# Performance work log

Measured on AMD Instinct MI355X. Metric: run time of the kernel, lower is better.

## Reference

```python
import jax, jax.numpy as jnp
import numpy as np

B = 64       # graphs per batch
NPG = 1000   # nodes per graph
EPG = 8000   # edges per graph
F = 128      # num_node_features


def _lin_w(k, fi, fo):
    s = 1.0 / np.sqrt(fi)
    return jax.random.uniform(k, (fi, fo), jnp.float32, -s, s)


def setup_inputs() -> dict:
    key = jax.random.key(0)
    ks = jax.random.split(key, 40)
    N, E = B * NPG, B * EPG

    def edges(k1, k2):
        src = jax.random.randint(k1, (E,), 0, NPG)
        dst = jax.random.randint(k2, (E,), 0, NPG)
        off = (jnp.arange(E) // EPG) * NPG  # keep edges within each graph
        return jnp.stack([src + off, dst + off]).astype(jnp.int32)

    inp = {
        'x0': jax.random.normal(ks[0], (N, F), jnp.float32),
        'edge_attr0': jax.random.uniform(ks[1], (E, 4), jnp.float32),
        'edge_index0': edges(ks[2], ks[3]),
        'x1': jax.random.normal(ks[4], (N, F), jnp.float32),
        'edge_attr1': jax.random.uniform(ks[5], (E, 4), jnp.float32),
        'edge_index1': edges(ks[6], ks[7]),
        'batch0': (jnp.arange(N) // NPG).astype(jnp.int32),
        'batch1': (jnp.arange(N) // NPG).astype(jnp.int32),
        'num_graphs': B,
    }
    # GCNConv weights/biases (6 convs, all F->F)
    names = ['1A', '1B', '1C', '1D', '2', '3']
    for i, nm in enumerate(names):
        inp['W' + nm] = _lin_w(ks[8 + i], F, F)
        inp['b' + nm] = jnp.zeros((F,), jnp.float32)
    # SAGPooling score GNN (GraphConv: lin_rel with bias, lin_root no bias), 3F -> 1
    inp['Ws_rel'] = _lin_w(ks[20], 3 * F, 1)
    inp['bs_rel'] = jnp.zeros((1,), jnp.float32)
    inp['Ws_root'] = _lin_w(ks[21], 3 * F, 1)
    # MLP: 6F -> 32 -> 8 -> 2
    inp['Wm1'] = _lin_w(ks[22], 6 * F, 32)
    inp['bm1'] = jnp.zeros((32,), jnp.float32)
    inp['Wm2'] = _lin_w(ks[23], 32, 8)
    inp['bm2'] = jnp.zeros((8,), jnp.float32)
    inp['Wm3'] = _lin_w(ks[24], 8, 2)
    inp['bm3'] = jnp.zeros((2,), jnp.float32)
    return inp


def gcn_conv(x, W, b, row, col, ew):
    # PyG GCNConv: add self-loops (w=1), symmetric norm, gather->scatter-add
    N = x.shape[0]
    h = x @ W  # [N, F]
    sl = jnp.arange(N)
    row_f = jnp.concatenate([row, sl])
    col_f = jnp.concatenate([col, sl])
    w_f = jnp.concatenate([ew, jnp.ones((N,), x.dtype)])
    deg = jax.ops.segment_sum(w_f, col_f, num_segments=N)
    dinv = jnp.where(deg > 0, jax.lax.rsqrt(jnp.maximum(deg, 1e-12)), 0.0)
    norm = (dinv[row_f] * w_f * dinv[col_f])[:, None]
    return jax.ops.segment_sum(h[row_f] * norm, col_f, num_segments=N) + b


def reference(x0, edge_attr0, edge_index0, x1, edge_attr1, edge_index1,
              batch0, batch1, num_graphs,
              W1A, b1A, W1B, b1B, W1C, b1C, W1D, b1D, W2, b2, W3, b3,
              Ws_rel, bs_rel, Ws_root, Wm1, bm1, Wm2, bm2, Wm3, bm3):
    Bn = int(num_graphs)

    def branch(x, ea, ei):
        row, col = ei[0], ei[1]
        N = x.shape[0]
        ones_e = jnp.ones((ei.shape[1],), x.dtype)
        xa = jax.nn.relu(gcn_conv(x, W1A, b1A, row, col, ea[:, 0]))
        xb = jax.nn.relu(gcn_conv(x, W1B, b1B, row, col, ea[:, 1]))
        xc = jax.nn.relu(gcn_conv(x, W1C, b1C, row, col, ea[:, 2]))
        xd = jax.nn.relu(gcn_conv(x, W1D, b1D, row, col, ea[:, 3]))
        g1 = (xa + xb + xc + xd) * 0.25
        g2 = jax.nn.relu(gcn_conv(g1, W2, b2, row, col, ones_e))
        g3 = gcn_conv(g2, W3, b3, row, col, ones_e)
        g = jnp.concatenate([g1, g2, g3], axis=1)  # [N, 3F]
        # SAGPooling score via GraphConv (sum aggr, no norm/self-loops)
        agg = jax.ops.segment_sum(g[row], col, num_segments=N)
        score = (agg @ Ws_rel + bs_rel + g @ Ws_root)[:, 0]  # [N]
        npg = N // Bn
        k = npg // 2  # ratio=0.5, even graph size
        sv, si = jax.lax.top_k(score.reshape(Bn, npg), k)
        gg = g.reshape(Bn, npg, g.shape[1])
        sel = jnp.take_along_axis(gg, si[..., None], axis=1)  # [B, k, 3F]
        pooled = sel * jnp.tanh(sv)[..., None]
        return pooled.mean(axis=1)  # global_mean_pool -> [B, 3F]

    r0 = branch(x0, edge_attr0, edge_index0)
    r1 = branch(x1, edge_attr1, edge_index1)
    r = jnp.concatenate([r0, r1], axis=1)  # [B, 6F]
    h = jax.nn.relu(r @ Wm1 + bm1)
    h = jax.nn.relu(h @ Wm2 + bm2)
    return h @ Wm3 + bm3  # [B, 2]
```

## Files before the change

kernel.cpp:

```cpp
#include <hip/hip_runtime.h>
#include <math.h>


#define TPB 256

__device__ __forceinline__ int swz_block(int bid, int nb) {
  int per = nb >> 3;
  return (bid & 7) * per + (bid >> 3);
}

__device__ __forceinline__ void f4fma(float4& a, const float4 b, float s) {
  a.x += b.x * s; a.y += b.y * s; a.z += b.z * s; a.w += b.w * s;
}
__device__ __forceinline__ float4 f4s(const float4 a, float s) {
  return make_float4(a.x * s, a.y * s, a.z * s, a.w * s);
}

__global__ __launch_bounds__(TPB) void count_k(const int* __restrict__ col,
                                               int* __restrict__ cnt, int E) {
  int e = blockIdx.x * TPB + threadIdx.x;
  if (e < E) atomicAdd(&cnt[col[e]], 1);
}

__global__ __launch_bounds__(TPB) void scan1_k(const int* __restrict__ cnt,
                                               int* __restrict__ rowptr,
                                               int* __restrict__ bsum, int N) {
  __shared__ int s[TPB];
  int tid = threadIdx.x;
  int gid = blockIdx.x * TPB + tid;
  int v = (gid < N) ? cnt[gid] : 0;
  s[tid] = v;
  __syncthreads();
  for (int o = 1; o < TPB; o <<= 1) {
    int t = (tid >= o) ? s[tid - o] : 0;
    __syncthreads();
    s[tid] += t;
    __syncthreads();
  }
  if (gid < N) rowptr[gid] = s[tid] - v;
  if (tid == TPB - 1) bsum[blockIdx.x] = s[TPB - 1];
}

__global__ __launch_bounds__(TPB) void scan2_k(int* __restrict__ bsum, int nb) {
  __shared__ int s[TPB];
  int tid = threadIdx.x;
  int v = (tid < nb) ? bsum[tid] : 0;
  s[tid] = v;
  __syncthreads();
  for (int o = 1; o < TPB; o <<= 1) {
    int t = (tid >= o) ? s[tid - o] : 0;
    __syncthreads();
    s[tid] += t;
    __syncthreads();
  }
  if (tid < nb) bsum[tid] = s[tid] - v;
}

__global__ __launch_bounds__(TPB) void scan3_k(int* __restrict__ rowptr,
                                               const int* __restrict__ bsum,
                                               int N, int E) {
  int gid = blockIdx.x * TPB + threadIdx.x;
  if (gid < N) rowptr[gid] += bsum[blockIdx.x];
  if (gid == 0) rowptr[N] = E;
}

__global__ __launch_bounds__(TPB) void fill_k(const int* __restrict__ col,
                                              const int* __restrict__ rowptr,
                                              int* __restrict__ fil,
                                              int* __restrict__ csr, int E) {
  int e = blockIdx.x * TPB + threadIdx.x;
  if (e < E) {
    int c = col[e];
    int p = rowptr[c] + atomicAdd(&fil[c], 1);
    csr[p] = e;
  }
}

__global__ __launch_bounds__(TPB) void sortadj_k(const int* __restrict__ rowptr,
                                                 int* __restrict__ csr, int N) {
  int i = blockIdx.x * TPB + threadIdx.x;
  if (i >= N) return;
  int s = rowptr[i], e = rowptr[i + 1];
  for (int a = s + 1; a < e; ++a) {
    int v = csr[a];
    int b = a - 1;
    while (b >= s && csr[b] > v) { csr[b + 1] = csr[b]; --b; }
    csr[b + 1] = v;
  }
}

__global__ __launch_bounds__(TPB) void deg_k(const int* __restrict__ rowptr,
                                             const int* __restrict__ csr,
                                             const float* __restrict__ ea,
                                             float* __restrict__ dinv, int N) {
  int i = blockIdx.x * TPB + threadIdx.x;
  if (i >= N) return;
  int s = rowptr[i], e = rowptr[i + 1];
  float d0 = 1.f, d1 = 1.f, d2 = 1.f, d3 = 1.f;
  for (int j = s; j < e; ++j) {
    int eid = csr[j];
    float4 w = *reinterpret_cast<const float4*>(&ea[(size_t)eid * 4]);
    d0 += w.x; d1 += w.y; d2 += w.z; d3 += w.w;
  }
  float dO = (float)(e - s) + 1.f;
  dinv[0 * N + i] = 1.f / sqrtf(d0);
  dinv[1 * N + i] = 1.f / sqrtf(d1);
  dinv[2 * N + i] = 1.f / sqrtf(d2);
  dinv[3 * N + i] = 1.f / sqrtf(d3);
  dinv[4 * N + i] = 1.f / sqrtf(dO);
}

__global__ __launch_bounds__(TPB) void eresolve_k(
    const int* __restrict__ csr, const int* __restrict__ erow,
    const float* __restrict__ ea, const float* __restrict__ dinv, int N, int E,
    int* __restrict__ csrSrc, float4* __restrict__ csrW,
    float* __restrict__ csrWO) {
  int j = blockIdx.x * TPB + threadIdx.x;
  if (j >= E) return;
  int eid = csr[j];
  int r = erow[eid];
  float4 a = *reinterpret_cast<const float4*>(&ea[(size_t)eid * 4]);
  csrSrc[j] = r;
  csrW[j] = make_float4(a.x * dinv[r], a.y * dinv[N + r], a.z * dinv[2 * N + r],
                        a.w * dinv[3 * N + r]);
  csrWO[j] = dinv[4 * N + r];
}

__global__ __launch_bounds__(256) void gather4_k(
    const float4* __restrict__ X, const int* __restrict__ rowptr,
    const int* __restrict__ csrSrc, const float4* __restrict__ csrW,
    const float* __restrict__ dinv, int N, float4* __restrict__ S0,
    float4* __restrict__ S1, float4* __restrict__ S2, float4* __restrict__ S3) {
  int sb = swz_block(blockIdx.x, gridDim.x);
  int node = sb * 8 + (threadIdx.x >> 5);
  int l = threadIdx.x & 31;
  int s = rowptr[node], e = rowptr[node + 1];
  float d0 = dinv[node], d1 = dinv[N + node], d2 = dinv[2 * N + node],
        d3 = dinv[3 * N + node];
  float4 xs = X[(size_t)node * 32 + l];
  float4 a0 = f4s(xs, d0), a1 = f4s(xs, d1), a2 = f4s(xs, d2), a3 = f4s(xs, d3);
  int j = s;
  for (; j + 3 < e; j += 4) {
    int r0 = csrSrc[j], r1 = csrSrc[j + 1], r2 = csrSrc[j + 2], r3 = csrSrc[j + 3];
    float4 w0 = csrW[j], w1 = csrW[j + 1], w2 = csrW[j + 2], w3 = csrW[j + 3];
    float4 x0 = X[(size_t)r0 * 32 + l];
    float4 x1 = X[(size_t)r1 * 32 + l];
    float4 x2 = X[(size_t)r2 * 32 + l];
    float4 x3 = X[(size_t)r3 * 32 + l];
    f4fma(a0, x0, w0.x); f4fma(a1, x0, w0.y); f4fma(a2, x0, w0.z); f4fma(a3, x0, w0.w);
    f4fma(a0, x1, w1.x); f4fma(a1, x1, w1.y); f4fma(a2, x1, w1.z); f4fma(a3, x1, w1.w);
    f4fma(a0, x2, w2.x); f4fma(a1, x2, w2.y); f4fma(a2, x2, w2.z); f4fma(a3, x2, w2.w);
    f4fma(a0, x3, w3.x); f4fma(a1, x3, w3.y); f4fma(a2, x3, w3.z); f4fma(a3, x3, w3.w);
  }
  for (; j < e; ++j) {
    int r = csrSrc[j];
    float4 w = csrW[j];
    float4 xr = X[(size_t)r * 32 + l];
    f4fma(a0, xr, w.x); f4fma(a1, xr, w.y); f4fma(a2, xr, w.z); f4fma(a3, xr, w.w);
  }
  size_t o = (size_t)node * 32 + l;
  S0[o] = f4s(a0, d0);
  S1[o] = f4s(a1, d1);
  S2[o] = f4s(a2, d2);
  S3[o] = f4s(a3, d3);
}

__global__ __launch_bounds__(256) void gather1_k(
    const float4* __restrict__ X, const int* __restrict__ rowptr,
    const int* __restrict__ csrSrc, const float* __restrict__ csrWO,
    const float* __restrict__ dinvO, int N, float4* __restrict__ Out) {
  int sb = swz_block(blockIdx.x, gridDim.x);
  int node = sb * 8 + (threadIdx.x >> 5);
  int l = threadIdx.x & 31;
  int s = rowptr[node], e = rowptr[node + 1];
  float di = dinvO[node];
  float4 acc = f4s(X[(size_t)node * 32 + l], di);
  int j = s;
  for (; j + 3 < e; j += 4) {
    int r0 = csrSrc[j], r1 = csrSrc[j + 1], r2 = csrSrc[j + 2], r3 = csrSrc[j + 3];
    float w0 = csrWO[j], w1 = csrWO[j + 1], w2 = csrWO[j + 2], w3 = csrWO[j + 3];
    float4 x0 = X[(size_t)r0 * 32 + l];
    float4 x1 = X[(size_t)r1 * 32 + l];
    float4 x2 = X[(size_t)r2 * 32 + l];
    float4 x3 = X[(size_t)r3 * 32 + l];
    f4fma(acc, x0, w0); f4fma(acc, x1, w1); f4fma(acc, x2, w2); f4fma(acc, x3, w3);
  }
  for (; j < e; ++j) {
    f4fma(acc, X[(size_t)csrSrc[j] * 32 + l], csrWO[j]);
  }
  Out[(size_t)node * 32 + l] = f4s(acc, di);
}

#define GEMM_STAGE(Aptr)                                                        \
  {                                                                             \
    _Pragma("unroll")                                                           \
    for (int i = 0; i < 4; ++i) {                                               \
      int u = tid + i * 256;                                                    \
      int r = u >> 3, k4 = u & 7;                                               \
      float4 v = *reinterpret_cast<const float4*>(                              \
          &Aptr[(size_t)(rowBase + r) * 128 + kc + k4 * 4]);                    \
      AsT[k4 * 4 + 0][r] = v.x;                                                 \
      AsT[k4 * 4 + 1][r] = v.y;                                                 \
      AsT[k4 * 4 + 2][r] = v.z;                                                 \
      AsT[k4 * 4 + 3][r] = v.w;                                                 \
    }                                                                           \
    _Pragma("unroll")                                                           \
    for (int i = 0; i < 4; ++i) {                                               \
      int u = tid + i * 256;                                                    \
      int r = u >> 5, c4 = u & 31;                                              \
      *reinterpret_cast<float4*>(&Ws[r][c4 * 4]) =                              \
          *reinterpret_cast<const float4*>(&Wp[(size_t)(kc + r) * 128 + c4 * 4]);\
    }                                                                           \
  }

#define GEMM_COMPUTE()                                                          \
  _Pragma("unroll 8")                                                           \
  for (int k = 0; k < 32; ++k) {                                                \
    float a[8], b[8];                                                           \
    *reinterpret_cast<float4*>(&a[0]) =                                         \
        *reinterpret_cast<const float4*>(&AsT[k][ty * 8]);                      \
    *reinterpret_cast<float4*>(&a[4]) =                                         \
        *reinterpret_cast<const float4*>(&AsT[k][ty * 8 + 4]);                  \
    *reinterpret_cast<float4*>(&b[0]) =                                         \
        *reinterpret_cast<const float4*>(&Ws[k][tx * 8]);                       \
    *reinterpret_cast<float4*>(&b[4]) =                                         \
        *reinterpret_cast<const float4*>(&Ws[k][tx * 8 + 4]);                   \
    _Pragma("unroll")                                                           \
    for (int j = 0; j < 8; ++j) {                                               \
      _Pragma("unroll")                                                         \
      for (int c = 0; c < 8; ++c) acc[j][c] += a[j] * b[c];                     \
    }                                                                           \
  }

template <bool RELU>
__global__ __launch_bounds__(256) void gemm_epi(const float* __restrict__ A,
                                                const float* __restrict__ Wp,
                                                const float* __restrict__ bias,
                                                float* __restrict__ C, int M) {
  __shared__ float AsT[32][132];
  __shared__ float Ws[32][128];
  int tid = threadIdx.x;
  int tx = tid & 15;
  int ty = tid >> 4;
  int rowBase = blockIdx.x * 128;
  float acc[8][8] = {};
  for (int kc = 0; kc < 128; kc += 32) {
    GEMM_STAGE(A);
    __syncthreads();
    GEMM_COMPUTE();
    __syncthreads();
  }
  float bb[8];
  *reinterpret_cast<float4*>(&bb[0]) = *reinterpret_cast<const float4*>(&bias[tx * 8]);
  *reinterpret_cast<float4*>(&bb[4]) = *reinterpret_cast<const float4*>(&bias[tx * 8 + 4]);
#pragma unroll
  for (int j = 0; j < 8; ++j) {
    float o[8];
#pragma unroll
    for (int c = 0; c < 8; ++c) {
      float v = acc[j][c] + bb[c];
      o[c] = RELU ? fmaxf(v, 0.f) : v;
    }
    size_t r = (size_t)(rowBase + ty * 8 + j) * 128 + tx * 8;
    *reinterpret_cast<float4*>(&C[r]) = *reinterpret_cast<float4*>(&o[0]);
    *reinterpret_cast<float4*>(&C[r + 4]) = *reinterpret_cast<float4*>(&o[4]);
  }
}

__global__ __launch_bounds__(256) void gemm4_k(
    const float* __restrict__ S0, const float* __restrict__ S1,
    const float* __restrict__ S2, const float* __restrict__ S3,
    const float* __restrict__ W0, const float* __restrict__ W1,
    const float* __restrict__ W2, const float* __restrict__ W3,
    const float* __restrict__ B0, const float* __restrict__ B1,
    const float* __restrict__ B2, const float* __restrict__ B3,
    float* __restrict__ g1, int M) {
  __shared__ float AsT[32][132];
  __shared__ float Ws[32][128];
  const float* Sarr[4] = {S0, S1, S2, S3};
  const float* Warr[4] = {W0, W1, W2, W3};
  const float* Barr[4] = {B0, B1, B2, B3};
  int tid = threadIdx.x;
  int tx = tid & 15;
  int ty = tid >> 4;
  int rowBase = blockIdx.x * 128;
  float facc[8][8] = {};
  for (int q = 0; q < 4; ++q) {
    const float* A = Sarr[q];
    const float* Wp = Warr[q];
    float acc[8][8] = {};
    for (int kc = 0; kc < 128; kc += 32) {
      GEMM_STAGE(A);
      __syncthreads();
      GEMM_COMPUTE();
      __syncthreads();
    }
    float bb[8];
    *reinterpret_cast<float4*>(&bb[0]) =
        *reinterpret_cast<const float4*>(&Barr[q][tx * 8]);
    *reinterpret_cast<float4*>(&bb[4]) =
        *reinterpret_cast<const float4*>(&Barr[q][tx * 8 + 4]);
#pragma unroll
    for (int j = 0; j < 8; ++j)
#pragma unroll
      for (int c = 0; c < 8; ++c)
        facc[j][c] += fmaxf(acc[j][c] + bb[c], 0.f) * 0.25f;
  }
#pragma unroll
  for (int j = 0; j < 8; ++j) {
    size_t r = (size_t)(rowBase + ty * 8 + j) * 128 + tx * 8;
    *reinterpret_cast<float4*>(&g1[r]) = *reinterpret_cast<float4*>(&facc[j][0]);
    *reinterpret_cast<float4*>(&g1[r + 4]) = *reinterpret_cast<float4*>(&facc[j][4]);
  }
}

__global__ __launch_bounds__(256) void score_a(
    const float* __restrict__ g1, const float* __restrict__ g2,
    const float* __restrict__ g3, const float* __restrict__ Wrel,
    const float* __restrict__ Wroot, float* __restrict__ trel,
    float* __restrict__ troot, int N) {
  int wave = threadIdx.x >> 6;
  int lane = threadIdx.x & 63;
  int node = blockIdx.x * 4 + wave;
  if (node >= N) return;
  float sr = 0.f, so = 0.f;
#pragma unroll
  for (int t = 0; t < 2; ++t) {
    int f = lane + t * 64;
    float v1 = g1[(size_t)node * 128 + f];
    float v2 = g2[(size_t)node * 128 + f];
    float v3 = g3[(size_t)node * 128 + f];
    sr += v1 * Wrel[f] + v2 * Wrel[128 + f] + v3 * Wrel[256 + f];
    so += v1 * Wroot[f] + v2 * Wroot[128 + f] + v3 * Wroot[256 + f];
  }
  for (int off = 32; off; off >>= 1) {
    sr += __shfl_down(sr, off);
    so += __shfl_down(so, off);
  }
  if (lane == 0) { trel[node] = sr; troot[node] = so; }
}

__global__ __launch_bounds__(TPB) void score_b(
    const int* __restrict__ rowptr, const int* __restrict__ csrSrc,
    const float* __restrict__ trel, const float* __restrict__ troot,
    const float* __restrict__ bs, float* __restrict__ score, int N) {
  int i = blockIdx.x * TPB + threadIdx.x;
  if (i >= N) return;
  float sc = bs[0] + troot[i];
  int s = rowptr[i], e = rowptr[i + 1];
  for (int j = s; j < e; ++j) sc += trel[csrSrc[j]];
  score[i] = sc;
}

__global__ __launch_bounds__(512) void topk_pool(
    const float* __restrict__ score, const float* __restrict__ g1,
    const float* __restrict__ g2, const float* __restrict__ g3,
    float* __restrict__ r, int half, int npg, int k) {
  __shared__ float key[1024];
  __shared__ int idx[1024];
  __shared__ float wts[512];
  int b = blockIdx.x;
  int tid = threadIdx.x;
  int base = b * npg;
  for (int i = tid; i < 1024; i += 512) {
    key[i] = (i < npg) ? score[base + i] : -3.0e38f;
    idx[i] = i;
  }
  __syncthreads();
  for (int kk = 2; kk <= 1024; kk <<= 1) {
    for (int j = kk >> 1; j > 0; j >>= 1) {
      for (int i = tid; i < 1024; i += 512) {
        int ixj = i ^ j;
        if (ixj > i) {
          bool desc = ((i & kk) == 0);
          float ki = key[i], kj = key[ixj];
          bool sw = desc ? (ki < kj) : (ki > kj);
          if (sw) {
            key[i] = kj; key[ixj] = ki;
            int t = idx[i]; idx[i] = idx[ixj]; idx[ixj] = t;
          }
        }
      }
      __syncthreads();
    }
  }
  if (tid < k) wts[tid] = tanhf(key[tid]);
  __syncthreads();
  if (tid < 384) {
    const float* gp = (tid < 128) ? g1 : ((tid < 256) ? g2 : g3);
    int fo = tid & 127;
    float acc = 0.f;
    for (int j = 0; j < k; ++j) {
      int n = base + idx[j];
      acc += wts[j] * gp[(size_t)n * 128 + fo];
    }
    r[(size_t)b * 768 + half * 384 + tid] = acc / (float)k;
  }
}

__global__ __launch_bounds__(64) void mlp_k(
    const float* __restrict__ r, const float* __restrict__ Wm1,
    const float* __restrict__ bm1, const float* __restrict__ Wm2,
    const float* __restrict__ bm2, const float* __restrict__ Wm3,
    const float* __restrict__ bm3, float* __restrict__ out) {
  __shared__ float rr[768];
  __shared__ float h1[32];
  __shared__ float h2[8];
  int b = blockIdx.x;
  int tid = threadIdx.x;
  for (int i = tid; i < 768; i += 64) rr[i] = r[(size_t)b * 768 + i];
  __syncthreads();
  if (tid < 32) {
    float s = bm1[tid];
    for (int i = 0; i < 768; ++i) s += rr[i] * Wm1[i * 32 + tid];
    h1[tid] = fmaxf(s, 0.f);
  }
  __syncthreads();
  if (tid < 8) {
    float s = bm2[tid];
    for (int i = 0; i < 32; ++i) s += h1[i] * Wm2[i * 8 + tid];
    h2[tid] = fmaxf(s, 0.f);
  }
  __syncthreads();
  if (tid < 2) {
    float s = bm3[tid];
    for (int i = 0; i < 8; ++i) s += h2[i] * Wm3[i * 2 + tid];
    out[b * 2 + tid] = s;
  }
}

extern "C" void kernel_launch(void* const* d_in, const int* in_sizes, int n_in,
                              void* d_out, int out_size, void* d_ws, size_t ws_size,
                              hipStream_t stream) {
  const float* x[2]  = {(const float*)d_in[0], (const float*)d_in[3]};
  const float* eat[2] = {(const float*)d_in[1], (const float*)d_in[4]};
  const int*   ei[2] = {(const int*)d_in[2], (const int*)d_in[5]};
  const int N = in_sizes[0] / 128;
  const int E = in_sizes[2] / 2;
  const int Bg = 64;
  const int npg = N / Bg;
  const int kq = npg / 2;

  const float* W1[4] = {(const float*)d_in[9], (const float*)d_in[11],
                        (const float*)d_in[13], (const float*)d_in[15]};
  const float* b1[4] = {(const float*)d_in[10], (const float*)d_in[12],
                        (const float*)d_in[14], (const float*)d_in[16]};
  const float* W2 = (const float*)d_in[17];
  const float* b2 = (const float*)d_in[18];
  const float* W3 = (const float*)d_in[19];
  const float* b3 = (const float*)d_in[20];
  const float* Wsrel  = (const float*)d_in[21];
  const float* bsrel  = (const float*)d_in[22];
  const float* Wsroot = (const float*)d_in[23];
  const float* Wm1 = (const float*)d_in[24];
  const float* bm1 = (const float*)d_in[25];
  const float* Wm2 = (const float*)d_in[26];
  const float* bm2 = (const float*)d_in[27];
  const float* Wm3 = (const float*)d_in[28];
  const float* bm3 = (const float*)d_in[29];
  float* out = (float*)d_out;

  char* ws = (char*)d_ws;
  size_t off = 0;
  auto alloc = [&](size_t bytes) -> void* {
    void* p = ws + off;
    off = (off + bytes + 511) & ~(size_t)511;
    return p;
  };
  const size_t nf = (size_t)N * 128 * sizeof(float);
  float* P0 = (float*)alloc(nf);
  float* P1 = (float*)alloc(nf);
  float* P2 = (float*)alloc(nf);
  float* P3 = (float*)alloc(nf);
  float* P4 = (float*)alloc(nf);
  float* dinv = (float*)alloc((size_t)5 * N * sizeof(float));
  float* trel = (float*)alloc((size_t)N * sizeof(float));
  float* trot = (float*)alloc((size_t)N * sizeof(float));
  float* sco  = (float*)alloc((size_t)N * sizeof(float));
  int* rowptr = (int*)alloc((size_t)(N + 1) * sizeof(int));
  int* cnt    = (int*)alloc((size_t)N * sizeof(int));
  int* csr    = (int*)alloc((size_t)E * sizeof(int));
  int* csrSrc = (int*)alloc((size_t)E * sizeof(int));
  float4* csrW = (float4*)alloc((size_t)E * sizeof(float4));
  float* csrWO = (float*)alloc((size_t)E * sizeof(float));
  int* bsum   = (int*)alloc(1024);
  float* rbuf = (float*)alloc((size_t)Bg * 768 * sizeof(float));
  if (off > ws_size) return;

  const int nbN = (N + TPB - 1) / TPB;
  const int nbE = (E + TPB - 1) / TPB;
  const int nbGather = N / 8;
  const int nbGemm = N / 128;

  for (int br = 0; br < 2; ++br) {
    const int* erow = ei[br];
    const int* ecol = ei[br] + E;

    hipMemsetAsync(cnt, 0, (size_t)N * sizeof(int), stream);
    count_k<<<nbE, TPB, 0, stream>>>(ecol, cnt, E);
    scan1_k<<<nbN, TPB, 0, stream>>>(cnt, rowptr, bsum, N);
    scan2_k<<<1, TPB, 0, stream>>>(bsum, nbN);
    scan3_k<<<nbN, TPB, 0, stream>>>(rowptr, bsum, N, E);
    hipMemsetAsync(cnt, 0, (size_t)N * sizeof(int), stream);
    fill_k<<<nbE, TPB, 0, stream>>>(ecol, rowptr, cnt, csr, E);
    sortadj_k<<<nbN, TPB, 0, stream>>>(rowptr, csr, N);
    deg_k<<<nbN, TPB, 0, stream>>>(rowptr, csr, eat[br], dinv, N);
    eresolve_k<<<nbE, TPB, 0, stream>>>(csr, erow, eat[br], dinv, N, E,
                                        csrSrc, csrW, csrWO);

    gather4_k<<<nbGather, 256, 0, stream>>>(
        (const float4*)x[br], rowptr, csrSrc, csrW, dinv, N,
        (float4*)P0, (float4*)P1, (float4*)P2, (float4*)P3);
    gemm4_k<<<nbGemm, 256, 0, stream>>>(P0, P1, P2, P3,
                                        W1[0], W1[1], W1[2], W1[3],
                                        b1[0], b1[1], b1[2], b1[3], P4, N);

    gather1_k<<<nbGather, 256, 0, stream>>>(
        (const float4*)P4, rowptr, csrSrc, csrWO, dinv + (size_t)4 * N, N,
        (float4*)P0);
    gemm_epi<true><<<nbGemm, 256, 0, stream>>>(P0, W2, b2, P1, N);

    gather1_k<<<nbGather, 256, 0, stream>>>(
        (const float4*)P1, rowptr, csrSrc, csrWO, dinv + (size_t)4 * N, N,
        (float4*)P0);
    gemm_epi<false><<<nbGemm, 256, 0, stream>>>(P0, W3, b3, P2, N);

    score_a<<<(N + 3) / 4, 256, 0, stream>>>(P4, P1, P2, Wsrel, Wsroot, trel, trot, N);
    score_b<<<nbN, TPB, 0, stream>>>(rowptr, csrSrc, trel, trot, bsrel, sco, N);
    topk_pool<<<Bg, 512, 0, stream>>>(sco, P4, P1, P2, rbuf, br, npg, kq);
  }

  mlp_k<<<Bg, 64, 0, stream>>>(rbuf, Wm1, bm1, Wm2, bm2, Wm3, bm3, out);
}
```

Measured before the change: 963.6 us.

## Double-buffer GEMM shared tiles with register prefetch and split thread-tile mapping

Rewrites the two dense GEMM kernels to double-buffer the A and W shared-memory tiles and prefetch the next K-chunk into registers while computing the current one. This halves the barriers per K step and hides global load latency. The per-thread 8x8 output tile is also split into two 4-wide halves 64 apart, which changes the shared-memory read pattern to cut LDS bank conflicts. Shared memory doubles per block and register pressure rises, which may lower occupancy.

```diff
diff --git a/kernel.cpp b/kernel.cpp
--- a/kernel.cpp
+++ b/kernel.cpp
@@ -191,79 +191,121 @@
   Out[(size_t)node * 32 + l] = f4s(acc, di);
 }
 
-#define GEMM_STAGE(Aptr)                                                        \
-  {                                                                             \
-    _Pragma("unroll")                                                           \
-    for (int i = 0; i < 4; ++i) {                                               \
-      int u = tid + i * 256;                                                    \
-      int r = u >> 3, k4 = u & 7;                                               \
-      float4 v = *reinterpret_cast<const float4*>(                              \
-          &Aptr[(size_t)(rowBase + r) * 128 + kc + k4 * 4]);                    \
-      AsT[k4 * 4 + 0][r] = v.x;                                                 \
-      AsT[k4 * 4 + 1][r] = v.y;                                                 \
-      AsT[k4 * 4 + 2][r] = v.z;                                                 \
-      AsT[k4 * 4 + 3][r] = v.w;                                                 \
-    }                                                                           \
-    _Pragma("unroll")                                                           \
-    for (int i = 0; i < 4; ++i) {                                               \
-      int u = tid + i * 256;                                                    \
-      int r = u >> 5, c4 = u & 31;                                              \
-      *reinterpret_cast<float4*>(&Ws[r][c4 * 4]) =                              \
-          *reinterpret_cast<const float4*>(&Wp[(size_t)(kc + r) * 128 + c4 * 4]);\
-    }                                                                           \
-  }
-
-#define GEMM_COMPUTE()                                                          \
-  _Pragma("unroll 8")                                                           \
-  for (int k = 0; k < 32; ++k) {                                                \
-    float a[8], b[8];                                                           \
-    *reinterpret_cast<float4*>(&a[0]) =                                         \
-        *reinterpret_cast<const float4*>(&AsT[k][ty * 8]);                      \
-    *reinterpret_cast<float4*>(&a[4]) =                                         \
-        *reinterpret_cast<const float4*>(&AsT[k][ty * 8 + 4]);                  \
-    *reinterpret_cast<float4*>(&b[0]) =                                         \
-        *reinterpret_cast<const float4*>(&Ws[k][tx * 8]);                       \
-    *reinterpret_cast<float4*>(&b[4]) =                                         \
-        *reinterpret_cast<const float4*>(&Ws[k][tx * 8 + 4]);                   \
-    _Pragma("unroll")                                                           \
-    for (int j = 0; j < 8; ++j) {                                               \
-      _Pragma("unroll")                                                         \
-      for (int c = 0; c < 8; ++c) acc[j][c] += a[j] * b[c];                     \
-    }                                                                           \
-  }
+
+__device__ __forceinline__ void g_loadA(const float* __restrict__ A, int rowBase,
+                                        int kc, int tid, float4* pa) {
+#pragma unroll
+  for (int i = 0; i < 4; ++i) {
+    int u = tid + i * 256;
+    int r = u >> 3, k4 = u & 7;
+    pa[i] = *reinterpret_cast<const float4*>(
+        &A[(size_t)(rowBase + r) * 128 + kc + k4 * 4]);
+  }
+}
+
+__device__ __forceinline__ void g_loadW(const float* __restrict__ W, int kc,
+                                        int tid, float4* pw) {
+#pragma unroll
+  for (int i = 0; i < 4; ++i) {
+    int u = tid + i * 256;
+    int r = u >> 5, c4 = u & 31;
+    pw[i] = *reinterpret_cast<const float4*>(&W[(size_t)(kc + r) * 128 + c4 * 4]);
+  }
+}
+
+__device__ __forceinline__ void s_store(float (*__restrict__ AsT)[130],
+                                        float (*__restrict__ Ws)[128], int tid,
+                                        const float4* pa, const float4* pw) {
+#pragma unroll
+  for (int i = 0; i < 4; ++i) {
+    int u = tid + i * 256;
+    int r = u >> 3, k4 = u & 7;
+    AsT[k4 * 4 + 0][r] = pa[i].x;
+    AsT[k4 * 4 + 1][r] = pa[i].y;
+    AsT[k4 * 4 + 2][r] = pa[i].z;
+    AsT[k4 * 4 + 3][r] = pa[i].w;
+    int r2 = u >> 5, c4 = u & 31;
+    *reinterpret_cast<float4*>(&Ws[r2][c4 * 4]) = pw[i];
+  }
+}
+
+__device__ __forceinline__ void compute32(const float (*__restrict__ AsT)[130],
+                                          const float (*__restrict__ Ws)[128],
+                                          int tx, int ty, float acc[8][8]) {
+#pragma unroll 8
+  for (int k = 0; k < 32; ++k) {
+    float a[8], b[8];
+    *reinterpret_cast<float4*>(&a[0]) =
+        *reinterpret_cast<const float4*>(&AsT[k][ty * 4]);
+    *reinterpret_cast<float4*>(&a[4]) =
+        *reinterpret_cast<const float4*>(&AsT[k][64 + ty * 4]);
+    *reinterpret_cast<float4*>(&b[0]) =
+        *reinterpret_cast<const float4*>(&Ws[k][tx * 4]);
+    *reinterpret_cast<float4*>(&b[4]) =
+        *reinterpret_cast<const float4*>(&Ws[k][64 + tx * 4]);
+#pragma unroll
+    for (int jr = 0; jr < 8; ++jr)
+#pragma unroll
+      for (int jc = 0; jc < 8; ++jc) acc[jr][jc] += a[jr] * b[jc];
+  }
+}
+
+__device__ __forceinline__ void gemm_pass(const float* __restrict__ A,
+                                          const float* __restrict__ W,
+                                          float (*__restrict__ AsT)[32][130],
+                                          float (*__restrict__ Ws)[32][128],
+                                          int rowBase, int tid, int tx, int ty,
+                                          float acc[8][8]) {
+  float4 pa[4], pw[4];
+  g_loadA(A, rowBase, 0, tid, pa);
+  g_loadW(W, 0, tid, pw);
+  s_store(AsT[0], Ws[0], tid, pa, pw);
+  g_loadA(A, rowBase, 32, tid, pa);
+  g_loadW(W, 32, tid, pw);
+#pragma unroll
+  for (int i = 0; i < 4; ++i) {
+    __syncthreads();
+    if (i < 3) {
+      s_store(AsT[(i + 1) & 1], Ws[(i + 1) & 1], tid, pa, pw);
+      if (i < 2) {
+        g_loadA(A, rowBase, (i + 2) * 32, tid, pa);
+        g_loadW(W, (i + 2) * 32, tid, pw);
+      }
+    }
+    compute32(AsT[i & 1], Ws[i & 1], tx, ty, acc);
+  }
+}
 
 template <bool RELU>
 __global__ __launch_bounds__(256) void gemm_epi(const float* __restrict__ A,
                                                 const float* __restrict__ Wp,
                                                 const float* __restrict__ bias,
                                                 float* __restrict__ C, int M) {
-  __shared__ float AsT[32][132];
-  __shared__ float Ws[32][128];
+  __shared__ float AsT[2][32][130];
+  __shared__ float Ws[2][32][128];
   int tid = threadIdx.x;
   int tx = tid & 15;
   int ty = tid >> 4;
   int rowBase = blockIdx.x * 128;
   float acc[8][8] = {};
-  for (int kc = 0; kc < 128; kc += 32) {
-    GEMM_STAGE(A);
-    __syncthreads();
-    GEMM_COMPUTE();
-    __syncthreads();
-  }
+  gemm_pass(A, Wp, AsT, Ws, rowBase, tid, tx, ty, acc);
   float bb[8];
-  *reinterpret_cast<float4*>(&bb[0]) = *reinterpret_cast<const float4*>(&bias[tx * 8]);
-  *reinterpret_cast<float4*>(&bb[4]) = *reinterpret_cast<const float4*>(&bias[tx * 8 + 4]);
-#pragma unroll
-  for (int j = 0; j < 8; ++j) {
+  *reinterpret_cast<float4*>(&bb[0]) = *reinterpret_cast<const float4*>(&bias[tx * 4]);
+  *reinterpret_cast<float4*>(&bb[4]) =
+      *reinterpret_cast<const float4*>(&bias[64 + tx * 4]);
+#pragma unroll
+  for (int jr = 0; jr < 8; ++jr) {
+    int row = rowBase + ((jr < 4) ? (ty * 4 + jr) : (64 + ty * 4 + jr - 4));
     float o[8];
 #pragma unroll
-    for (int c = 0; c < 8; ++c) {
-      float v = acc[j][c] + bb[c];
-      o[c] = RELU ? fmaxf(v, 0.f) : v;
+    for (int jc = 0; jc < 8; ++jc) {
+      float v = acc[jr][jc] + bb[jc];
+      o[jc] = RELU ? fmaxf(v, 0.f) : v;
     }
-    size_t r = (size_t)(rowBase + ty * 8 + j) * 128 + tx * 8;
-    *reinterpret_cast<float4*>(&C[r]) = *reinterpret_cast<float4*>(&o[0]);
-    *reinterpret_cast<float4*>(&C[r + 4]) = *reinterpret_cast<float4*>(&o[4]);
+    *reinterpret_cast<float4*>(&C[(size_t)row * 128 + tx * 4]) =
+        *reinterpret_cast<float4*>(&o[0]);
+    *reinterpret_cast<float4*>(&C[(size_t)row * 128 + 64 + tx * 4]) =
+        *reinterpret_cast<float4*>(&o[4]);
   }
 }
 
@@ -275,8 +317,8 @@
     const float* __restrict__ B0, const float* __restrict__ B1,
     const float* __restrict__ B2, const float* __restrict__ B3,
     float* __restrict__ g1, int M) {
-  __shared__ float AsT[32][132];
-  __shared__ float Ws[32][128];
+  __shared__ float AsT[2][32][130];
+  __shared__ float Ws[2][32][128];
   const float* Sarr[4] = {S0, S1, S2, S3};
   const float* Warr[4] = {W0, W1, W2, W3};
   const float* Barr[4] = {B0, B1, B2, B3};
@@ -286,31 +328,27 @@
   int rowBase = blockIdx.x * 128;
   float facc[8][8] = {};
   for (int q = 0; q < 4; ++q) {
-    const float* A = Sarr[q];
-    const float* Wp = Warr[q];
     float acc[8][8] = {};
-    for (int kc = 0; kc < 128; kc += 32) {
-      GEMM_STAGE(A);
-      __syncthreads();
-      GEMM_COMPUTE();
-      __syncthreads();
-    }
+    gemm_pass(Sarr[q], Warr[q], AsT, Ws, rowBase, tid, tx, ty, acc);
     float bb[8];
     *reinterpret_cast<float4*>(&bb[0]) =
-        *reinterpret_cast<const float4*>(&Barr[q][tx * 8]);
+        *reinterpret_cast<const float4*>(&Barr[q][tx * 4]);
     *reinterpret_cast<float4*>(&bb[4]) =
-        *reinterpret_cast<const float4*>(&Barr[q][tx * 8 + 4]);
-#pragma unroll
-    for (int j = 0; j < 8; ++j)
-#pragma unroll
-      for (int c = 0; c < 8; ++c)
-        facc[j][c] += fmaxf(acc[j][c] + bb[c], 0.f) * 0.25f;
-  }
-#pragma unroll
-  for (int j = 0; j < 8; ++j) {
-    size_t r = (size_t)(rowBase + ty * 8 + j) * 128 + tx * 8;
-    *reinterpret_cast<float4*>(&g1[r]) = *reinterpret_cast<float4*>(&facc[j][0]);
-    *reinterpret_cast<float4*>(&g1[r + 4]) = *reinterpret_cast<float4*>(&facc[j][4]);
+        *reinterpret_cast<const float4*>(&Barr[q][64 + tx * 4]);
+#pragma unroll
+    for (int jr = 0; jr < 8; ++jr)
+#pragma unroll
+      for (int jc = 0; jc < 8; ++jc)
+        facc[jr][jc] += fmaxf(acc[jr][jc] + bb[jc], 0.f) * 0.25f;
+    __syncthreads();
+  }
+#pragma unroll
+  for (int jr = 0; jr < 8; ++jr) {
+    int row = rowBase + ((jr < 4) ? (ty * 4 + jr) : (64 + ty * 4 + jr - 4));
+    *reinterpret_cast<float4*>(&g1[(size_t)row * 128 + tx * 4]) =
+        *reinterpret_cast<float4*>(&facc[jr][0]);
+    *reinterpret_cast<float4*>(&g1[(size_t)row * 128 + 64 + tx * 4]) =
+        *reinterpret_cast<float4*>(&facc[jr][4]);
   }
 }
 
```

Measured after the change: 1.192 ms. +23.7%, slower.
